# Kernel optimization log

Measured on AMD Instinct MI355X. Metric: run time of the kernel, lower is better.

Reference implementation:

```python
import jax, jax.numpy as jnp
import numpy as np

N = [40000, 120000, 80000, 20000]   # simplices per rank 0..3
C = 128
OUT = 10
L = 2
ADJ_NNZ = [320000, 960000, 640000, 160000]
INC_NNZ = [240000, 240000, 80000]   # incidence ranks 1..3


def setup_inputs() -> dict:
    key = jax.random.key(0)
    ki = iter(jax.random.split(key, 40))
    inp = {}
    for r in range(4):
        inp[f"x{r}"] = jax.random.normal(next(ki), (N[r], C), dtype=jnp.float32)
    for r in range(4):
        inp[f"adj{r}_row"] = jax.random.randint(next(ki), (ADJ_NNZ[r],), 0, N[r], dtype=jnp.int32)
        inp[f"adj{r}_col"] = jax.random.randint(next(ki), (ADJ_NNZ[r],), 0, N[r], dtype=jnp.int32)
        inp[f"adj{r}_val"] = jax.random.normal(next(ki), (ADJ_NNZ[r],), dtype=jnp.float32) * 0.1
    for r in range(1, 4):
        nnz = INC_NNZ[r - 1]
        inp[f"inc{r}_row"] = jax.random.randint(next(ki), (nnz,), 0, N[r - 1], dtype=jnp.int32)
        inp[f"inc{r}_col"] = jax.random.randint(next(ki), (nnz,), 0, N[r], dtype=jnp.int32)
        inp[f"inc{r}_val"] = jax.random.normal(next(ki), (nnz,), dtype=jnp.float32) * 0.1
    s = 1.0 / np.sqrt(C).astype(np.float32)
    inp["W_same"] = jax.random.normal(next(ki), (L, 4, C, C), dtype=jnp.float32) * s
    inp["W_h2l"] = jax.random.normal(next(ki), (L, 3, C, C), dtype=jnp.float32) * s
    inp["W_l2h"] = jax.random.normal(next(ki), (L, 3, C, C), dtype=jnp.float32) * s
    inp["W_out"] = jax.random.normal(next(ki), (C, OUT), dtype=jnp.float32) * s
    inp["b_out"] = jnp.zeros((OUT,), dtype=jnp.float32)
    return inp


def _spmm(row, col, val, x, n_rows):
    # y[i] = sum_{k: row[k]==i} val[k] * x[col[k]]   (sparse COO @ dense)
    return jax.ops.segment_sum(val[:, None] * x[col], row, num_segments=n_rows)


def _sccn_forward(xs, adj, inc, W_same, W_h2l, W_l2h):
    for l in range(L):
        new_xs = []
        for r in range(4):
            row, col, val = adj[r]
            m = _spmm(row, col, val, xs[r] @ W_same[l, r], N[r])
            if r < 3:  # high-to-low: incidence_{r+1} @ (x_{r+1} W)
                irow, icol, ival = inc[r]
                m = m + _spmm(irow, icol, ival, xs[r + 1] @ W_h2l[l, r], N[r])
            if r > 0:  # low-to-high: incidence_r^T @ (x_{r-1} W)
                irow, icol, ival = inc[r - 1]
                m = m + _spmm(icol, irow, ival, xs[r - 1] @ W_l2h[l, r - 1], N[r])
            new_xs.append(jax.nn.sigmoid(m))  # update_func='sigmoid' after sum-aggregation
        xs = new_xs
    return xs


def reference(x0, x1, x2, x3,
              adj0_row, adj0_col, adj0_val,
              adj1_row, adj1_col, adj1_val,
              adj2_row, adj2_col, adj2_val,
              adj3_row, adj3_col, adj3_val,
              inc1_row, inc1_col, inc1_val,
              inc2_row, inc2_col, inc2_val,
              inc3_row, inc3_col, inc3_val,
              W_same, W_h2l, W_l2h, W_out, b_out):
    adj = [(adj0_row, adj0_col, adj0_val), (adj1_row, adj1_col, adj1_val),
           (adj2_row, adj2_col, adj2_val), (adj3_row, adj3_col, adj3_val)]
    inc = [(inc1_row, inc1_col, inc1_val), (inc2_row, inc2_col, inc2_val),
           (inc3_row, inc3_col, inc3_val)]
    xs = _sccn_forward([x0, x1, x2, x3], adj, inc, W_same, W_h2l, W_l2h)
    logits = xs[0] @ W_out + b_out
    return jax.nn.softmax(logits, axis=1)
```

## Files before the change

kernel.cpp:

```cpp
#include <hip/hip_runtime.h>

#define CH 128
#define EPB 2048
#define RPB 512
#define MAXBUK 1024
#define MAXBLK 2048

typedef __attribute__((ext_vector_type(8))) short short8;
typedef __attribute__((ext_vector_type(4))) float floatx4;

__device__ __forceinline__ float bf2f(unsigned short u) {
    union { unsigned int i; float f; } v; v.i = ((unsigned int)u) << 16; return v.f;
}
__device__ __forceinline__ unsigned short f2bf(float f) {
    union { float f; unsigned int i; } v; v.f = f;
    unsigned int r = v.i + 0x7FFF + ((v.i >> 16) & 1);
    return (unsigned short)(r >> 16);
}


__global__ __launch_bounds__(256) void k_wt_all(const float* __restrict__ Ws,
                                                const float* __restrict__ Wh,
                                                const float* __restrict__ Wl,
                                                unsigned short* __restrict__ WT) {
    int i = blockIdx.x * 256 + threadIdx.x;
    if (i >= (20 << 14)) return;
    int mat = i >> 14, rem = i & 16383;
    int k = rem >> 7, n = rem & 127;
    float w;
    if (mat < 8)       w = Ws[(mat << 14) + rem];
    else if (mat < 14) w = Wh[((mat - 8) << 14) + rem];
    else               w = Wl[((mat - 14) << 14) + rem];
    WT[(mat << 14) + (n << 7) + k] = f2bf(w);
}


struct Segs {
    const int*   row[10];
    const int*   col[10];
    const float* val[10];
    int base[10];
    int coff[10];
    int nnz[10];
    int start[10];
};

__device__ __forceinline__ int seg_of(const Segs& sg, int blk) {
    int s = 0;
    for (int k = 1; k < 10; ++k) if (blk >= sg.start[k]) s = k;
    return s;
}

__global__ __launch_bounds__(256) void k_bkt_count(Segs sg, int nbuk, int* __restrict__ M) {
    __shared__ int lcnt[MAXBUK];
    int s = seg_of(sg, blockIdx.x);
    int t = threadIdx.x;
    int b0 = (blockIdx.x - sg.start[s]) * EPB;
    int nnz = sg.nnz[s];
    const int* __restrict__ rowp = sg.row[s];
    int sbase = sg.base[s];
    for (int j = t; j < nbuk; j += 256) lcnt[j] = 0;
    __syncthreads();
#pragma unroll
    for (int k = 0; k < 8; ++k) {
        int i = b0 + k * 256 + t;
        if (i < nnz) atomicAdd(&lcnt[(sbase + rowp[i]) >> 9], 1);
    }
    __syncthreads();
    int* Mr = M + (size_t)blockIdx.x * nbuk;
    for (int j = t; j < nbuk; j += 256) Mr[j] = lcnt[j];
}

__global__ __launch_bounds__(256) void k_colscan(int* __restrict__ M, int nblk, int nbuk,
                                                 int* __restrict__ colsum) {
    __shared__ int a[2][MAXBLK];
    int b = blockIdx.x, t = threadIdx.x;
    for (int j = t; j < MAXBLK; j += 256) a[0][j] = (j < nblk) ? M[(size_t)j * nbuk + b] : 0;
    __syncthreads();
    int src = 0;
    for (int off = 1; off < MAXBLK; off <<= 1) {
        for (int j = t; j < MAXBLK; j += 256) {
            int v = a[src][j];
            if (j >= off) v += a[src][j - off];
            a[src ^ 1][j] = v;
        }
        __syncthreads();
        src ^= 1;
    }
    for (int j = t; j < nblk; j += 256)
        M[(size_t)j * nbuk + b] = (j == 0) ? 0 : a[src][j - 1];
    if (t == 0) colsum[b] = a[src][nblk - 1];
}

__global__ __launch_bounds__(256) void k_bkt_scan(const int* __restrict__ colsum, int nbuk,
                                                  int* __restrict__ bucketBase,
                                                  int* __restrict__ rowptr_last) {
    __shared__ int a[2][MAXBUK];
    int t = threadIdx.x;
    for (int j = t; j < MAXBUK; j += 256) a[0][j] = (j < nbuk) ? colsum[j] : 0;
    __syncthreads();
    int src = 0;
    for (int off = 1; off < MAXBUK; off <<= 1) {
        for (int j = t; j < MAXBUK; j += 256) {
            int v = a[src][j];
            if (j >= off) v += a[src][j - off];
            a[src ^ 1][j] = v;
        }
        __syncthreads();
        src ^= 1;
    }
    for (int j = t; j < nbuk; j += 256) bucketBase[j] = (j == 0) ? 0 : a[src][j - 1];
    if (t == 0) { bucketBase[nbuk] = a[src][nbuk - 1]; *rowptr_last = a[src][nbuk - 1]; }
}

__global__ __launch_bounds__(256) void k_bkt_scatter(Segs sg, int nbuk,
                                                     const int* __restrict__ M,
                                                     const int* __restrict__ bucketBase,
                                                     int2* __restrict__ bcv) {
    __shared__ int lcnt[MAXBUK];
    __shared__ int lbase[MAXBUK];
    int s = seg_of(sg, blockIdx.x);
    int t = threadIdx.x;
    int b0 = (blockIdx.x - sg.start[s]) * EPB;
    int nnz = sg.nnz[s];
    const int* __restrict__ rowp = sg.row[s];
    const int* __restrict__ colp = sg.col[s];
    const float* __restrict__ valp = sg.val[s];
    int sbase = sg.base[s];
    int scoff = sg.coff[s];
    for (int j = t; j < nbuk; j += 256) lcnt[j] = 0;
    __syncthreads();
    int rank[8], grow[8];
#pragma unroll
    for (int k = 0; k < 8; ++k) {
        int i = b0 + k * 256 + t;
        if (i < nnz) {
            grow[k] = sbase + rowp[i];
            rank[k] = atomicAdd(&lcnt[grow[k] >> 9], 1);
        }
    }
    __syncthreads();
    const int* Mr = M + (size_t)blockIdx.x * nbuk;
    for (int j = t; j < nbuk; j += 256) lbase[j] = bucketBase[j] + Mr[j];
    __syncthreads();
#pragma unroll
    for (int k = 0; k < 8; ++k) {
        int i = b0 + k * 256 + t;
        if (i < nnz) {
            int pos = lbase[grow[k] >> 9] + rank[k];
            int packed = ((grow[k] & (RPB - 1)) << 19) | (colp[i] + scoff);
            bcv[pos] = make_int2(packed, __float_as_int(valp[i]));
        }
    }
}

__global__ __launch_bounds__(256) void k_bkt_csr(const int2* __restrict__ bcv,
                                                 const int* __restrict__ bucketBase,
                                                 int* __restrict__ rowptr, int totalRows,
                                                 int2* __restrict__ edg) {
    __shared__ int ptr[RPB];
    __shared__ int swt[4];
    int b = blockIdx.x, t = threadIdx.x;
    int bb = bucketBase[b], be = bucketBase[b + 1];
    int bsz = be - bb;
    int rowLo = b << 9;
    for (int j = t; j < RPB; j += 256) ptr[j] = 0;
    __syncthreads();
    for (int i = t; i < bsz; i += 256)
        atomicAdd(&ptr[((unsigned)bcv[bb + i].x) >> 19], 1);
    __syncthreads();
    int base2 = t * 2;
    int c[2];
    int s = 0;
#pragma unroll
    for (int k = 0; k < 2; ++k) { c[k] = ptr[base2 + k]; s += c[k]; }
    int lane = t & 63, w = t >> 6;
    int incl = s;
    for (int off = 1; off < 64; off <<= 1) {
        int u = __shfl_up(incl, off, 64);
        if (lane >= off) incl += u;
    }
    if (lane == 63) swt[w] = incl;
    __syncthreads();
    int waveoff = 0;
    for (int k = 0; k < w; ++k) waveoff += swt[k];
    int run = waveoff + incl - s;
    int nrv = totalRows - rowLo; if (nrv > RPB) nrv = RPB;
#pragma unroll
    for (int k = 0; k < 2; ++k) {
        int j = base2 + k;
        ptr[j] = run;
        if (j < nrv) rowptr[rowLo + j] = bb + run;
        run += c[k];
    }
    __syncthreads();
    for (int i = t; i < bsz; i += 256) {
        int2 e = bcv[bb + i];
        int lrow = ((unsigned)e.x) >> 19;
        int pos = atomicAdd(&ptr[lrow], 1);
        edg[bb + pos] = make_int2(e.x & 0x7FFFF, e.y);
    }
}


__device__ __forceinline__ int lds_idx(int r, int koff) {
    return (r << 7) + ((((koff >> 3) ^ (r & 15))) << 3);
}

__device__ __forceinline__ void gemm_core(const unsigned short* sA, const unsigned short* sB,
                                          unsigned short* __restrict__ Y, int M, int row0, int t) {
    const int wave = t >> 6;
    const int lane = t & 63;
    const int quad = lane >> 4;
    const int l16  = lane & 15;
    const int rbase = wave * 32;

    floatx4 acc[2][8];
    for (int i = 0; i < 2; ++i)
        for (int j = 0; j < 8; ++j) acc[i][j] = (floatx4){0.f, 0.f, 0.f, 0.f};

    for (int kk = 0; kk < 4; ++kk) {
        int ko = kk * 32 + quad * 8;
        short8 a0 = *(const short8*)(&sA[lds_idx(rbase + l16, ko)]);
        short8 a1 = *(const short8*)(&sA[lds_idx(rbase + 16 + l16, ko)]);
        for (int j = 0; j < 8; ++j) {
            short8 b = *(const short8*)(&sB[lds_idx(j * 16 + l16, ko)]);
            acc[0][j] = __builtin_amdgcn_mfma_f32_16x16x32_bf16(a0, b, acc[0][j], 0, 0, 0);
            acc[1][j] = __builtin_amdgcn_mfma_f32_16x16x32_bf16(a1, b, acc[1][j], 0, 0, 0);
        }
    }

    for (int i = 0; i < 2; ++i) {
        int rg0 = row0 + rbase + i * 16 + quad * 4;
        for (int reg = 0; reg < 4; ++reg) {
            int rg = rg0 + reg;
            if (rg >= M) continue;
            unsigned short* yr = Y + (size_t)rg * CH;
            for (int j = 0; j < 8; ++j)
                yr[j * 16 + l16] = f2bf(acc[i][j][reg]);
        }
    }
}

struct GJobs {
    const void* A[3];
    const unsigned short* Bt[3];
    unsigned short* Y[3];
    int M[3];
    int bstart[4];
    int njobs;
};

__global__ __launch_bounds__(256) void k_gemm_multi(GJobs g) {
    __shared__ __align__(16) unsigned short sA[128 * 128];
    __shared__ __align__(16) unsigned short sB[128 * 128];
    const int t = threadIdx.x;
    int b = blockIdx.x;
    int j = 0;
    if (g.njobs > 1 && b >= g.bstart[1]) j = 1;
    if (g.njobs > 2 && b >= g.bstart[2]) j = 2;
    const unsigned short* A = (const unsigned short*)g.A[j];
    const unsigned short* Bt = g.Bt[j];
    unsigned short* Y = g.Y[j];
    int M = g.M[j];
    const int row0 = (b - g.bstart[j]) * 128;

    for (int it = 0; it < 8; ++it) {
        int chunk = it * 256 + t;
        int r = chunk >> 4;
        int cidx = chunk & 15;
        int coff = cidx << 3;
        int sidx = (r << 7) + (((cidx ^ (r & 15))) << 3);
        *(float4*)(&sB[sidx]) = *(const float4*)(Bt + (r << 7) + coff);
        int gr = row0 + r;
        float4 av = make_float4(0.f, 0.f, 0.f, 0.f);
        if (gr < M) av = *(const float4*)(A + (size_t)gr * CH + coff);
        *(float4*)(&sA[sidx]) = av;
    }
    __syncthreads();
    gemm_core(sA, sB, Y, M, row0, t);
}

__global__ __launch_bounds__(256) void k_gemm_multi_f32(GJobs g) {
    __shared__ __align__(16) unsigned short sA[128 * 128];
    __shared__ __align__(16) unsigned short sB[128 * 128];
    const int t = threadIdx.x;
    int b = blockIdx.x;
    int j = 0;
    if (g.njobs > 1 && b >= g.bstart[1]) j = 1;
    if (g.njobs > 2 && b >= g.bstart[2]) j = 2;
    const float* A = (const float*)g.A[j];
    const unsigned short* Bt = g.Bt[j];
    unsigned short* Y = g.Y[j];
    int M = g.M[j];
    const int row0 = (b - g.bstart[j]) * 128;

    for (int it = 0; it < 8; ++it) {
        int chunk = it * 256 + t;
        int r = chunk >> 4;
        int cidx = chunk & 15;
        int coff = cidx << 3;
        int sidx = (r << 7) + (((cidx ^ (r & 15))) << 3);
        *(float4*)(&sB[sidx]) = *(const float4*)(Bt + (r << 7) + coff);
        int gr = row0 + r;
        unsigned short us[8];
        if (gr < M) {
            const float* ar = A + (size_t)gr * CH + coff;
            float4 f0 = *(const float4*)ar;
            float4 f1 = *(const float4*)(ar + 4);
            us[0] = f2bf(f0.x); us[1] = f2bf(f0.y); us[2] = f2bf(f0.z); us[3] = f2bf(f0.w);
            us[4] = f2bf(f1.x); us[5] = f2bf(f1.y); us[6] = f2bf(f1.z); us[7] = f2bf(f1.w);
        } else {
            for (int k = 0; k < 8; ++k) us[k] = 0;
        }
        *(float4*)(&sA[sidx]) = *(const float4*)us;
    }
    __syncthreads();
    gemm_core(sA, sB, Y, M, row0, t);
}


__device__ __forceinline__ void g_load(const int2* __restrict__ eg, int j, int n,
                                       const unsigned short* __restrict__ y, int coff,
                                       int2* e, unsigned int* u) {
#pragma unroll
    for (int k = 0; k < 8; ++k) {
        if (k < n) {
            e[k] = eg[j + k];
            u[k] = *(const unsigned int*)(y + (((size_t)(unsigned)e[k].x) << 7) + coff);
        }
    }
}

__device__ __forceinline__ void g_acc(const int2* e, const unsigned int* u, int n,
                                      float& a0, float& a1) {
#pragma unroll
    for (int k = 0; k < 8; ++k) {
        if (k < n) {
            float v = __int_as_float(e[k].y);
            a0 += v * __int_as_float(u[k] << 16);
            a1 += v * __int_as_float(u[k] & 0xffff0000u);
        }
    }
}

__global__ __launch_bounds__(256) void k_gather(
    const int* __restrict__ rp, const unsigned short* __restrict__ y,
    const int2* __restrict__ eArena,
    unsigned short* __restrict__ xout, int M)
{
    int wrow = blockIdx.x * 4 + (threadIdx.x >> 6);
    if (wrow >= M) return;
    wrow = __builtin_amdgcn_readfirstlane(wrow);
    int lane = threadIdx.x & 63;
    int coff = lane * 2;
    float a0 = 0.f, a1 = 0.f;

    int jb = __builtin_amdgcn_readfirstlane(rp[wrow]);
    int je = __builtin_amdgcn_readfirstlane(rp[wrow + 1]);
    int j = jb;
    int2 ea[8]; unsigned int ua[8];
    int2 eb[8]; unsigned int ub[8];
    int n0 = je - j; if (n0 > 8) n0 = 8;
    if (n0 > 0) g_load(eArena, j, n0, y, coff, ea, ua);
    j += n0;
    while (j < je) {
        int n1 = je - j; if (n1 > 8) n1 = 8;
        g_load(eArena, j, n1, y, coff, eb, ub);
        j += n1;
        g_acc(ea, ua, n0, a0, a1);
#pragma unroll
        for (int k = 0; k < 8; ++k) {
            if (k < n1) { ea[k] = eb[k]; ua[k] = ub[k]; }
        }
        n0 = n1;
    }
    if (n0 > 0) g_acc(ea, ua, n0, a0, a1);

    float s0 = 1.0f / (1.0f + __expf(-a0));
    float s1 = 1.0f / (1.0f + __expf(-a1));
    ushort2 o;
    o.x = f2bf(s0);
    o.y = f2bf(s1);
    *(ushort2*)(xout + (size_t)wrow * CH + coff) = o;
}


__global__ __launch_bounds__(128) void k_out(const unsigned short* __restrict__ x0,
                                             const float* __restrict__ Wout,
                                             const float* __restrict__ bout,
                                             float* __restrict__ out, int M) {
    __shared__ float sl[8][16];
    int rlocal = threadIdx.x >> 4;
    int o = threadIdx.x & 15;
    int rowi = blockIdx.x * 8 + rlocal;
    float acc = 0.f;
    if (rowi < M && o < 10) {
        const unsigned short* xr = x0 + (size_t)rowi * CH;
        for (int k = 0; k < CH; ++k)
            acc += bf2f(xr[k]) * Wout[k * 10 + o];
        acc += bout[o];
    }
    sl[rlocal][o] = acc;
    __syncthreads();
    if (rowi < M && o < 10) {
        float mx = -1e30f;
        for (int j = 0; j < 10; ++j) mx = fmaxf(mx, sl[rlocal][j]);
        float s = 0.f;
        for (int j = 0; j < 10; ++j) s += __expf(sl[rlocal][j] - mx);
        out[rowi * 10 + o] = __expf(sl[rlocal][o] - mx) / s;
    }
}


extern "C" void kernel_launch(void* const* d_in, const int* in_sizes, int n_in,
                              void* d_out, int out_size, void* d_ws, size_t ws_size,
                              hipStream_t stream) {
    const float* xin[4];
    for (int r = 0; r < 4; ++r) xin[r] = (const float*)d_in[r];
    const int* arow[4]; const int* acol[4]; const float* aval[4];
    for (int r = 0; r < 4; ++r) {
        arow[r] = (const int*)d_in[4 + 3 * r];
        acol[r] = (const int*)d_in[5 + 3 * r];
        aval[r] = (const float*)d_in[6 + 3 * r];
    }
    const int* irow[3]; const int* icol[3]; const float* ival[3];
    for (int r = 0; r < 3; ++r) {
        irow[r] = (const int*)d_in[16 + 3 * r];
        icol[r] = (const int*)d_in[17 + 3 * r];
        ival[r] = (const float*)d_in[18 + 3 * r];
    }
    const float* W_same = (const float*)d_in[25];
    const float* W_h2l  = (const float*)d_in[26];
    const float* W_l2h  = (const float*)d_in[27];
    const float* W_out  = (const float*)d_in[28];
    const float* b_out  = (const float*)d_in[29];

    int Nr[4], adjnnz[4], incnnz[3];
    for (int r = 0; r < 4; ++r) { Nr[r] = in_sizes[r] / CH; adjnnz[r] = in_sizes[4 + 3 * r]; }
    for (int r = 0; r < 3; ++r) incnnz[r] = in_sizes[16 + 3 * r];
    int Nmax = 0;
    for (int r = 0; r < 4; ++r) if (Nr[r] > Nmax) Nmax = Nr[r];
    size_t totalN = (size_t)Nr[0] + Nr[1] + Nr[2] + Nr[3];
    size_t totAdj = 0; for (int r = 0; r < 4; ++r) totAdj += adjnnz[r];
    size_t totInc = 0; for (int r = 0; r < 3; ++r) totInc += incnnz[r];
    size_t totEdges = totAdj + 2 * totInc;

    int baseRank[4];
    int acc_rows = 0;
    for (int r = 0; r < 4; ++r) { baseRank[r] = acc_rows; acc_rows += Nr[r]; }
    int totalRowsU = acc_rows;
    int nbuk = (totalRowsU + RPB - 1) >> 9;

    char* ws = (char*)d_ws;
    size_t off = 0;
    auto take = [&](size_t bytes) { char* p = ws + off; off += (bytes + 255) & ~(size_t)255; return p; };
    unsigned short* xbuf  = (unsigned short*)take(totalN * CH * 2);
    unsigned short* yS    = (unsigned short*)take((size_t)4 * Nmax * CH * 2);
    unsigned short* WT    = (unsigned short*)take((size_t)20 * 16384 * 2);
    int*  rowptrG= (int*)take(((size_t)totalRowsU + 1) * 4);
    int2* eArena = (int2*)take(totEdges * 8);
    (void)ws_size;

    unsigned short* yH  = yS + (size_t)Nmax * CH;
    unsigned short* yLe = yS + (size_t)2 * Nmax * CH;
    unsigned short* yLo = yS + (size_t)3 * Nmax * CH;
    unsigned short* yLslot[2] = { yLe, yLo };

    unsigned short* WsT = WT;
    unsigned short* WhT = WT + ((size_t)8 << 14);
    unsigned short* WlT = WT + ((size_t)14 << 14);

    unsigned short* x[4];
    {
        size_t o = 0;
        for (int r = 0; r < 4; ++r) { x[r] = xbuf + o; o += (size_t)Nr[r] * CH; }
    }

    Segs sg;
    int nblk = 0;
    {
        for (int r = 0; r < 4; ++r) {
            sg.row[r] = arow[r]; sg.col[r] = acol[r]; sg.val[r] = aval[r];
            sg.base[r] = baseRank[r]; sg.coff[r] = 0;
            sg.nnz[r] = adjnnz[r]; sg.start[r] = nblk;
            nblk += (adjnnz[r] + EPB - 1) / EPB;
        }
        for (int s = 0; s < 3; ++s) {
            sg.row[4 + s] = irow[s]; sg.col[4 + s] = icol[s]; sg.val[4 + s] = ival[s];
            sg.base[4 + s] = baseRank[s]; sg.coff[4 + s] = Nmax;
            sg.nnz[4 + s] = incnnz[s]; sg.start[4 + s] = nblk;
            nblk += (incnnz[s] + EPB - 1) / EPB;
        }
        for (int s = 0; s < 3; ++s) {
            sg.row[7 + s] = icol[s]; sg.col[7 + s] = irow[s]; sg.val[7 + s] = ival[s];
            sg.base[7 + s] = baseRank[s + 1];
            sg.coff[7 + s] = (2 + ((s + 1) & 1)) * Nmax;
            sg.nnz[7 + s] = incnnz[s]; sg.start[7 + s] = nblk;
            nblk += (incnnz[s] + EPB - 1) / EPB;
        }

        int2* bcv  = (int2*)yS;
        int*  M    = (int*)yLe;
        int*  colsum     = M + (size_t)nblk * nbuk;
        int*  bucketBase = colsum + nbuk;

        k_bkt_count  <<<nblk, 256, 0, stream>>>(sg, nbuk, M);
        k_colscan    <<<nbuk, 256, 0, stream>>>(M, nblk, nbuk, colsum);
        k_bkt_scan   <<<1,    256, 0, stream>>>(colsum, nbuk, bucketBase, rowptrG + totalRowsU);
        k_bkt_scatter<<<nblk, 256, 0, stream>>>(sg, nbuk, M, bucketBase, bcv);
        k_bkt_csr    <<<nbuk, 256, 0, stream>>>(bcv, bucketBase, rowptrG, totalRowsU, eArena);
    }

    k_wt_all<<<(20 * 16384 + 255) / 256, 256, 0, stream>>>(W_same, W_h2l, W_l2h, WT);

    for (int l = 0; l < 2; ++l) {
        for (int r = 0; r < 4; ++r) {
            GJobs g;
            int nj = 0;
            g.A[nj] = (l == 0) ? (const void*)xin[r] : (const void*)x[r];
            g.Bt[nj] = WsT + (((size_t)(l * 4 + r)) << 14);
            g.Y[nj] = yS; g.M[nj] = Nr[r];
            ++nj;
            if (r < 3) {
                g.A[nj] = (l == 0) ? (const void*)xin[r + 1] : (const void*)x[r + 1];
                g.Bt[nj] = WhT + (((size_t)(l * 3 + r)) << 14);
                g.Y[nj] = yH; g.M[nj] = Nr[r + 1];
                ++nj;
                g.A[nj] = (l == 0) ? (const void*)xin[r] : (const void*)x[r];
                g.Bt[nj] = WlT + (((size_t)(l * 3 + r)) << 14);
                g.Y[nj] = yLslot[(r + 1) & 1]; g.M[nj] = Nr[r];
                ++nj;
            }
            g.njobs = nj;
            int bacc = 0;
            for (int k = 0; k < nj; ++k) { g.bstart[k] = bacc; bacc += (g.M[k] + 127) / 128; }
            g.bstart[nj] = bacc;
            if (l == 0) k_gemm_multi_f32<<<bacc, 256, 0, stream>>>(g);
            else        k_gemm_multi    <<<bacc, 256, 0, stream>>>(g);

            k_gather<<<(Nr[r] + 3) / 4, 256, 0, stream>>>(
                rowptrG + baseRank[r], yS, eArena, x[r], Nr[r]);
        }
    }

    k_out<<<(Nr[0] + 7) / 8, 128, 0, stream>>>(x[0], W_out, b_out, (float*)d_out, Nr[0]);
}
```

Baseline: 832.9 us.

## Batch rank GEMMs and gathers into pairs using a slot-based Y arena

Replaces the per-rank GEMM+gather sequence (8 GEMM and 8 gather launches) with two batched GEMM launches of up to six jobs each and two gathers covering ranks 0-1 and 2-3 per layer. A new Y arena with even/odd slots per message type lets two ranks' projections coexist, and the CSR column offsets are remapped to those slots. Bucket size drops from 512 to 256 rows, so one row per thread in the CSR build and a 24-bit column field. This cuts launch count and tail underutilisation, at the cost of a larger workspace and tighter index packing limits.

```diff
diff --git a/kernel.cpp b/kernel.cpp
--- a/kernel.cpp
+++ b/kernel.cpp
@@ -2,7 +2,7 @@
 
 #define CH 128
 #define EPB 2048
-#define RPB 512
+#define RPB 256
 #define MAXBUK 1024
 #define MAXBLK 2048
 
@@ -64,7 +64,7 @@
 #pragma unroll
     for (int k = 0; k < 8; ++k) {
         int i = b0 + k * 256 + t;
-        if (i < nnz) atomicAdd(&lcnt[(sbase + rowp[i]) >> 9], 1);
+        if (i < nnz) atomicAdd(&lcnt[(sbase + rowp[i]) >> 8], 1);
     }
     __syncthreads();
     int* Mr = M + (size_t)blockIdx.x * nbuk;
@@ -136,7 +136,7 @@
         int i = b0 + k * 256 + t;
         if (i < nnz) {
             grow[k] = sbase + rowp[i];
-            rank[k] = atomicAdd(&lcnt[grow[k] >> 9], 1);
+            rank[k] = atomicAdd(&lcnt[grow[k] >> 8], 1);
         }
     }
     __syncthreads();
@@ -147,8 +147,8 @@
     for (int k = 0; k < 8; ++k) {
         int i = b0 + k * 256 + t;
         if (i < nnz) {
-            int pos = lbase[grow[k] >> 9] + rank[k];
-            int packed = ((grow[k] & (RPB - 1)) << 19) | (colp[i] + scoff);
+            int pos = lbase[grow[k] >> 8] + rank[k];
+            int packed = ((grow[k] & (RPB - 1)) << 24) | (colp[i] + scoff);
             bcv[pos] = make_int2(packed, __float_as_int(valp[i]));
         }
     }
@@ -163,19 +163,15 @@
     int b = blockIdx.x, t = threadIdx.x;
     int bb = bucketBase[b], be = bucketBase[b + 1];
     int bsz = be - bb;
-    int rowLo = b << 9;
-    for (int j = t; j < RPB; j += 256) ptr[j] = 0;
+    int rowLo = b << 8;
+    ptr[t] = 0;
     __syncthreads();
     for (int i = t; i < bsz; i += 256)
-        atomicAdd(&ptr[((unsigned)bcv[bb + i].x) >> 19], 1);
-    __syncthreads();
-    int base2 = t * 2;
-    int c[2];
-    int s = 0;
-#pragma unroll
-    for (int k = 0; k < 2; ++k) { c[k] = ptr[base2 + k]; s += c[k]; }
+        atomicAdd(&ptr[((unsigned)bcv[bb + i].x) >> 24], 1);
+    __syncthreads();
+    int c = ptr[t];
     int lane = t & 63, w = t >> 6;
-    int incl = s;
+    int incl = c;
     for (int off = 1; off < 64; off <<= 1) {
         int u = __shfl_up(incl, off, 64);
         if (lane >= off) incl += u;
@@ -184,21 +180,15 @@
     __syncthreads();
     int waveoff = 0;
     for (int k = 0; k < w; ++k) waveoff += swt[k];
-    int run = waveoff + incl - s;
-    int nrv = totalRows - rowLo; if (nrv > RPB) nrv = RPB;
-#pragma unroll
-    for (int k = 0; k < 2; ++k) {
-        int j = base2 + k;
-        ptr[j] = run;
-        if (j < nrv) rowptr[rowLo + j] = bb + run;
-        run += c[k];
-    }
+    int run = waveoff + incl - c;
+    ptr[t] = run;
+    if (rowLo + t < totalRows) rowptr[rowLo + t] = bb + run;
     __syncthreads();
     for (int i = t; i < bsz; i += 256) {
         int2 e = bcv[bb + i];
-        int lrow = ((unsigned)e.x) >> 19;
+        int lrow = ((unsigned)e.x) >> 24;
         int pos = atomicAdd(&ptr[lrow], 1);
-        edg[bb + pos] = make_int2(e.x & 0x7FFFF, e.y);
+        edg[bb + pos] = make_int2(e.x & 0x00FFFFFF, e.y);
     }
 }
 
@@ -243,11 +233,11 @@
 }
 
 struct GJobs {
-    const void* A[3];
-    const unsigned short* Bt[3];
-    unsigned short* Y[3];
-    int M[3];
-    int bstart[4];
+    const void* A[6];
+    const unsigned short* Bt[6];
+    unsigned short* Y[6];
+    int M[6];
+    int bstart[7];
     int njobs;
 };
 
@@ -257,8 +247,7 @@
     const int t = threadIdx.x;
     int b = blockIdx.x;
     int j = 0;
-    if (g.njobs > 1 && b >= g.bstart[1]) j = 1;
-    if (g.njobs > 2 && b >= g.bstart[2]) j = 2;
+    while (j + 1 < g.njobs && b >= g.bstart[j + 1]) ++j;
     const unsigned short* A = (const unsigned short*)g.A[j];
     const unsigned short* Bt = g.Bt[j];
     unsigned short* Y = g.Y[j];
@@ -287,8 +276,7 @@
     const int t = threadIdx.x;
     int b = blockIdx.x;
     int j = 0;
-    if (g.njobs > 1 && b >= g.bstart[1]) j = 1;
-    if (g.njobs > 2 && b >= g.bstart[2]) j = 2;
+    while (j + 1 < g.njobs && b >= g.bstart[j + 1]) ++j;
     const float* A = (const float*)g.A[j];
     const unsigned short* Bt = g.Bt[j];
     unsigned short* Y = g.Y[j];
@@ -439,8 +427,6 @@
     int Nr[4], adjnnz[4], incnnz[3];
     for (int r = 0; r < 4; ++r) { Nr[r] = in_sizes[r] / CH; adjnnz[r] = in_sizes[4 + 3 * r]; }
     for (int r = 0; r < 3; ++r) incnnz[r] = in_sizes[16 + 3 * r];
-    int Nmax = 0;
-    for (int r = 0; r < 4; ++r) if (Nr[r] > Nmax) Nmax = Nr[r];
     size_t totalN = (size_t)Nr[0] + Nr[1] + Nr[2] + Nr[3];
     size_t totAdj = 0; for (int r = 0; r < 4; ++r) totAdj += adjnnz[r];
     size_t totInc = 0; for (int r = 0; r < 3; ++r) totInc += incnnz[r];
@@ -450,22 +436,29 @@
     int acc_rows = 0;
     for (int r = 0; r < 4; ++r) { baseRank[r] = acc_rows; acc_rows += Nr[r]; }
     int totalRowsU = acc_rows;
-    int nbuk = (totalRowsU + RPB - 1) >> 9;
+    int nbuk = (totalRowsU + RPB - 1) >> 8;
+
+    auto imax = [](int a, int b) { return a > b ? a : b; };
+    int szSe = imax(Nr[0], Nr[2]), szSo = imax(Nr[1], Nr[3]);
+    int szHe = imax(Nr[1], Nr[3]), szHo = Nr[2];
+    int szLe = Nr[1],              szLo = imax(Nr[0], Nr[2]);
+    int bSe = 0;
+    int bSo = bSe + szSe;
+    int bHe = bSo + szSo;
+    int bHo = bHe + szHe;
+    int bLe = bHo + szHo;
+    int bLo = bLe + szLe;
+    int yRows = bLo + szLo;
 
     char* ws = (char*)d_ws;
     size_t off = 0;
     auto take = [&](size_t bytes) { char* p = ws + off; off += (bytes + 255) & ~(size_t)255; return p; };
-    unsigned short* xbuf  = (unsigned short*)take(totalN * CH * 2);
-    unsigned short* yS    = (unsigned short*)take((size_t)4 * Nmax * CH * 2);
-    unsigned short* WT    = (unsigned short*)take((size_t)20 * 16384 * 2);
-    int*  rowptrG= (int*)take(((size_t)totalRowsU + 1) * 4);
-    int2* eArena = (int2*)take(totEdges * 8);
+    unsigned short* xbuf   = (unsigned short*)take(totalN * CH * 2);
+    unsigned short* yArena = (unsigned short*)take((size_t)yRows * CH * 2);
+    unsigned short* WT     = (unsigned short*)take((size_t)20 * 16384 * 2);
+    int*  rowptrG = (int*)take(((size_t)totalRowsU + 1) * 4);
+    int2* eArena  = (int2*)take(totEdges * 8);
     (void)ws_size;
-
-    unsigned short* yH  = yS + (size_t)Nmax * CH;
-    unsigned short* yLe = yS + (size_t)2 * Nmax * CH;
-    unsigned short* yLo = yS + (size_t)3 * Nmax * CH;
-    unsigned short* yLslot[2] = { yLe, yLo };
 
     unsigned short* WsT = WT;
     unsigned short* WhT = WT + ((size_t)8 << 14);
@@ -482,26 +475,28 @@
     {
         for (int r = 0; r < 4; ++r) {
             sg.row[r] = arow[r]; sg.col[r] = acol[r]; sg.val[r] = aval[r];
-            sg.base[r] = baseRank[r]; sg.coff[r] = 0;
+            sg.base[r] = baseRank[r];
+            sg.coff[r] = (r & 1) ? bSo : bSe;
             sg.nnz[r] = adjnnz[r]; sg.start[r] = nblk;
             nblk += (adjnnz[r] + EPB - 1) / EPB;
         }
         for (int s = 0; s < 3; ++s) {
             sg.row[4 + s] = irow[s]; sg.col[4 + s] = icol[s]; sg.val[4 + s] = ival[s];
-            sg.base[4 + s] = baseRank[s]; sg.coff[4 + s] = Nmax;
+            sg.base[4 + s] = baseRank[s];
+            sg.coff[4 + s] = (s & 1) ? bHo : bHe;
             sg.nnz[4 + s] = incnnz[s]; sg.start[4 + s] = nblk;
             nblk += (incnnz[s] + EPB - 1) / EPB;
         }
         for (int s = 0; s < 3; ++s) {
             sg.row[7 + s] = icol[s]; sg.col[7 + s] = irow[s]; sg.val[7 + s] = ival[s];
             sg.base[7 + s] = baseRank[s + 1];
-            sg.coff[7 + s] = (2 + ((s + 1) & 1)) * Nmax;
+            sg.coff[7 + s] = ((s + 1) & 1) ? bLo : bLe;
             sg.nnz[7 + s] = incnnz[s]; sg.start[7 + s] = nblk;
             nblk += (incnnz[s] + EPB - 1) / EPB;
         }
 
-        int2* bcv  = (int2*)yS;
-        int*  M    = (int*)yLe;
+        int2* bcv = (int2*)yArena;
+        int*  M   = (int*)xbuf;
         int*  colsum     = M + (size_t)nblk * nbuk;
         int*  bucketBase = colsum + nbuk;
 
@@ -514,33 +509,55 @@
 
     k_wt_all<<<(20 * 16384 + 255) / 256, 256, 0, stream>>>(W_same, W_h2l, W_l2h, WT);
 
+    unsigned short* ySlotS[2] = { yArena + (size_t)bSe * CH, yArena + (size_t)bSo * CH };
+    unsigned short* ySlotH[2] = { yArena + (size_t)bHe * CH, yArena + (size_t)bHo * CH };
+    unsigned short* ySlotL[2] = { yArena + (size_t)bLe * CH, yArena + (size_t)bLo * CH };
+
     for (int l = 0; l < 2; ++l) {
-        for (int r = 0; r < 4; ++r) {
-            GJobs g;
-            int nj = 0;
-            g.A[nj] = (l == 0) ? (const void*)xin[r] : (const void*)x[r];
-            g.Bt[nj] = WsT + (((size_t)(l * 4 + r)) << 14);
-            g.Y[nj] = yS; g.M[nj] = Nr[r];
-            ++nj;
-            if (r < 3) {
-                g.A[nj] = (l == 0) ? (const void*)xin[r + 1] : (const void*)x[r + 1];
-                g.Bt[nj] = WhT + (((size_t)(l * 3 + r)) << 14);
-                g.Y[nj] = yH; g.M[nj] = Nr[r + 1];
-                ++nj;
-                g.A[nj] = (l == 0) ? (const void*)xin[r] : (const void*)x[r];
-                g.Bt[nj] = WlT + (((size_t)(l * 3 + r)) << 14);
-                g.Y[nj] = yLslot[(r + 1) & 1]; g.M[nj] = Nr[r];
-                ++nj;
-            }
+        auto Ain = [&](int r) -> const void* {
+            return (l == 0) ? (const void*)xin[r] : (const void*)x[r];
+        };
+        {
+            GJobs g; int nj = 0;
+            auto add = [&](const void* A, const unsigned short* Bt, unsigned short* Y, int M) {
+                g.A[nj] = A; g.Bt[nj] = Bt; g.Y[nj] = Y; g.M[nj] = M; ++nj;
+            };
+            add(Ain(0), WsT + (((size_t)(l * 4 + 0)) << 14), ySlotS[0], Nr[0]);
+            add(Ain(1), WhT + (((size_t)(l * 3 + 0)) << 14), ySlotH[0], Nr[1]);
+            add(Ain(0), WlT + (((size_t)(l * 3 + 0)) << 14), ySlotL[1], Nr[0]);
+            add(Ain(1), WsT + (((size_t)(l * 4 + 1)) << 14), ySlotS[1], Nr[1]);
+            add(Ain(2), WhT + (((size_t)(l * 3 + 1)) << 14), ySlotH[1], Nr[2]);
+            add(Ain(1), WlT + (((size_t)(l * 3 + 1)) << 14), ySlotL[0], Nr[1]);
             g.njobs = nj;
             int bacc = 0;
             for (int k = 0; k < nj; ++k) { g.bstart[k] = bacc; bacc += (g.M[k] + 127) / 128; }
             g.bstart[nj] = bacc;
             if (l == 0) k_gemm_multi_f32<<<bacc, 256, 0, stream>>>(g);
             else        k_gemm_multi    <<<bacc, 256, 0, stream>>>(g);
-
-            k_gather<<<(Nr[r] + 3) / 4, 256, 0, stream>>>(
-                rowptrG + baseRank[r], yS, eArena, x[r], Nr[r]);
+        }
+        {
+            int Mg = Nr[0] + Nr[1];
+            k_gather<<<(Mg + 3) / 4, 256, 0, stream>>>(rowptrG, yArena, eArena, xbuf, Mg);
+        }
+        {
+            GJobs g; int nj = 0;
+            auto add = [&](const void* A, const unsigned short* Bt, unsigned short* Y, int M) {
+                g.A[nj] = A; g.Bt[nj] = Bt; g.Y[nj] = Y; g.M[nj] = M; ++nj;
+            };
+            add(Ain(2), WsT + (((size_t)(l * 4 + 2)) << 14), ySlotS[0], Nr[2]);
+            add(Ain(3), WhT + (((size_t)(l * 3 + 2)) << 14), ySlotH[0], Nr[3]);
+            add(Ain(2), WlT + (((size_t)(l * 3 + 2)) << 14), ySlotL[1], Nr[2]);
+            add(Ain(3), WsT + (((size_t)(l * 4 + 3)) << 14), ySlotS[1], Nr[3]);
+            g.njobs = nj;
+            int bacc = 0;
+            for (int k = 0; k < nj; ++k) { g.bstart[k] = bacc; bacc += (g.M[k] + 127) / 128; }
+            g.bstart[nj] = bacc;
+            if (l == 0) k_gemm_multi_f32<<<bacc, 256, 0, stream>>>(g);
+            else        k_gemm_multi    <<<bacc, 256, 0, stream>>>(g);
+        }
+        {
+            int Mg = Nr[2] + Nr[3];
+            k_gather<<<(Mg + 3) / 4, 256, 0, stream>>>(rowptrG + baseRank[2], yArena, eArena, x[2], Mg);
         }
     }
 
```

After: 831.2 us. About the same (-0.2%).
